# Performance work log

Measured on AMD Instinct MI355X. Metric: run time of the kernel, lower is better.

The kernel has to match this reference:

```python
import jax, jax.numpy as jnp
import numpy as np

H = 4      # hidden_size
L = 5      # num_layers
IN = 1     # input_size
B = 1024   # batch
T = 2048   # seq_len


def setup_inputs() -> dict:
    key = jax.random.key(0)
    ks = jax.random.split(key, 6)
    s = 1.0 / np.sqrt(H)  # PyTorch LSTM init: U(-1/sqrt(H), 1/sqrt(H))
    u = lambda k, shape: jax.random.uniform(k, shape, jnp.float32, -s, s)
    return {
        "x": jax.random.normal(ks[0], (B, T, IN), jnp.float32),
        "w_ih0": u(ks[1], (4 * H, IN)),          # layer 0 input weights
        "w_ih_rest": u(ks[2], (L - 1, 4 * H, H)),  # layers 1..L-1 input weights
        "w_hh": u(ks[3], (L, 4 * H, H)),
        "b_ih": u(ks[4], (L, 4 * H)),
        "b_hh": u(ks[5], (L, 4 * H)),
    }


def _lstm_layer(seq, w_ih, w_hh, b_ih, b_hh):
    # seq: [T, B, in] -> outputs [T, B, H], final hidden [B, H]
    # Precompute input contributions for all timesteps (one big GEMM).
    gx = jnp.einsum('tbi,gi->tbg', seq, w_ih) + b_ih + b_hh  # [T, B, 4H]
    h0 = jnp.zeros((seq.shape[1], H), seq.dtype)
    c0 = h0

    def step(carry, g_t):
        h, c = carry
        g = g_t + h @ w_hh.T                      # [B, 4H]
        i, f, gc, o = jnp.split(g, 4, axis=-1)    # PyTorch gate order i,f,g,o
        i = jax.nn.sigmoid(i)
        f = jax.nn.sigmoid(f)
        o = jax.nn.sigmoid(o)
        c = f * c + i * jnp.tanh(gc)
        h = o * jnp.tanh(c)
        return (h, c), h

    (hT, _), out = jax.lax.scan(step, (h0, c0), gx)
    return out, hT


def reference(x, w_ih0, w_ih_rest, w_hh, b_ih, b_hh):
    seq = jnp.transpose(x, (1, 0, 2))  # batch_first -> time-major [T, B, IN]
    out, hT = _lstm_layer(seq, w_ih0, w_hh[0], b_ih[0], b_hh[0])
    for l in range(L - 1):  # fixed small layer count; structural loop is fine
        out, hT = _lstm_layer(out, w_ih_rest[l], w_hh[l + 1], b_ih[l + 1], b_hh[l + 1])
    # final hidden state of the last (top) layer == rnn_hidden_states[-1]
    return hT  # [B, H]
```

## Files before the change

kernel.cpp:

```cpp
#include <hip/hip_runtime.h>
#include <stdint.h>


#define T_LEN   2048
#define NLAYER  5
#define CHUNK   32
#define NCHUNK  (T_LEN / CHUNK)
#define NPHASE  (NCHUNK + NLAYER - 1)

template <int CTRL>
__device__ __forceinline__ float dppmov(float x) {
  int v = __builtin_amdgcn_mov_dpp(__float_as_int(x), CTRL, 0xF, 0xF, true);
  return __int_as_float(v);
}

template <bool STORE>
__device__ __forceinline__ void lstm_step(
    float gxv, const float* whh, float k1, float k0,
    float& hr0, float& hr1, float& hr2, float& hr3, float& c,
    float* __restrict__ slot)
{
  const float LOG2E = 1.4426950408889634f;

  float t01 = fmaf(whh[0], hr0, gxv);
  t01 = fmaf(whh[1], hr1, t01);
  float t23 = whh[2] * hr2;
  t23 = fmaf(whh[3], hr3, t23);
  const float acc = t01 + t23;

  const float E = __builtin_amdgcn_exp2f(acc);
  const float A = 1.f + E;
  const float R = __builtin_amdgcn_rcpf(A);
  const float act = fmaf(k1, R, k0);

  const float iv = dppmov<0x00>(act);
  const float fv = dppmov<0x55>(act);
  const float gv = dppmov<0xAA>(act);
  const float ov = dppmov<0xFF>(act);
  const float ov2 = ov + ov;
  const float ovm = -ov;

  c = fmaf(fv, c, iv * gv);
  const float ct = c * (-2.0f * LOG2E);
  const float E2 = __builtin_amdgcn_exp2f(ct);
  const float A2 = 1.f + E2;
  const float R2 = __builtin_amdgcn_rcpf(A2);
  const float h  = fmaf(ov2, R2, ovm);

  hr0 = h;
  hr1 = dppmov<0x124>(h);
  hr2 = dppmov<0x128>(h);
  hr3 = dppmov<0x12C>(h);

  if (STORE) *slot = h;
}

__global__ void __launch_bounds__(64 * NLAYER, 1) lstm_pipe(
    const float* __restrict__ x,
    const float* __restrict__ w_ih0,
    const float* __restrict__ w_ih_rest,
    const float* __restrict__ w_hh,
    const float* __restrict__ b_ih,
    const float* __restrict__ b_hh,
    float* __restrict__ out)
{
  const int tid  = threadIdx.x;
  const int l    = tid >> 6;
  const int lane = tid & 63;
  const int q    = lane & 15;
  const int el   = lane >> 4;
  const int e    = blockIdx.x * 4 + el;
  const int gt   = q & 3;
  const int j    = q >> 2;
  const int r    = gt * 4 + j;

  const float LOG2E = 1.4426950408889634f;
  const float s  = (gt == 2) ? (-2.0f * LOG2E) : (-LOG2E);
  const float k1 = (gt == 2) ? 2.0f : 1.0f;
  const float k0 = (gt == 2) ? -1.0f : 0.0f;

  float whh[4];
  float wih[4] = {0.f, 0.f, 0.f, 0.f};
  #pragma unroll
  for (int m = 0; m < 4; ++m) {
    const int k = (j - m) & 3;
    whh[m] = w_hh[l * 64 + r * 4 + k] * s;
  }
  if (l > 0) {
    #pragma unroll
    for (int m = 0; m < 4; ++m) {
      const int k = (j - m) & 3;
      wih[m] = w_ih_rest[(l - 1) * 64 + r * 4 + k] * s;
    }
  }
  float wx = 0.f;
  if (l == 0) wx = w_ih0[r] * s;
  const float bias = (b_ih[l * 16 + r] + b_hh[l * 16 + r]) * s;

  float hr0 = 0.f, hr1 = 0.f, hr2 = 0.f, hr3 = 0.f;
  float c = 0.f;

  __shared__ float buf[NLAYER - 1][2][CHUNK][4][16];

  float gx[CHUNK];
  float xcur[CHUNK];

  if (l == 0) {
    #pragma unroll
    for (int tc = 0; tc < CHUNK; ++tc) xcur[tc] = x[e * T_LEN + tc];
  }

  for (int p = 0; p < NPHASE; ++p) {
    const int n = p - l;
    if (n >= 0 && n < NCHUNK) {
      const int par = n & 1;

      if (l == 0) {
        #pragma unroll
        for (int tc = 0; tc < CHUNK; ++tc)
          gx[tc] = fmaf(wx, xcur[tc], bias);
        if (n + 1 < NCHUNK) {
          #pragma unroll
          for (int tc = 0; tc < CHUNK; ++tc)
            xcur[tc] = x[e * T_LEN + (n + 1) * CHUNK + tc];
        }
      } else {
        #pragma unroll
        for (int tc = 0; tc < CHUNK; ++tc) {
          const float a0 = buf[l - 1][par][tc][el][q];
          const float a1 = dppmov<0x124>(a0);
          const float a2 = dppmov<0x128>(a0);
          const float a3 = dppmov<0x12C>(a0);
          float acc = fmaf(wih[0], a0, bias);
          acc = fmaf(wih[1], a1, acc);
          float acc2 = wih[2] * a2;
          acc2 = fmaf(wih[3], a3, acc2);
          gx[tc] = acc + acc2;
        }
      }

      __builtin_amdgcn_s_setprio(1);
      if (l < NLAYER - 1) {
        float* slotbase = &buf[l][par][0][el][q];
        #pragma unroll
        for (int tc = 0; tc < CHUNK; ++tc)
          lstm_step<true>(gx[tc], whh, k1, k0, hr0, hr1, hr2, hr3, c,
                          slotbase + tc * 64);
      } else {
        #pragma unroll
        for (int tc = 0; tc < CHUNK; ++tc)
          lstm_step<false>(gx[tc], whh, k1, k0, hr0, hr1, hr2, hr3, c,
                           nullptr);
      }
      __builtin_amdgcn_s_setprio(0);

      if (l == NLAYER - 1 && n == NCHUNK - 1 && gt == 0) out[e * 4 + j] = hr0;
    }
    __syncthreads();
  }
}

extern "C" void kernel_launch(void* const* d_in, const int* in_sizes, int n_in,
                              void* d_out, int out_size, void* d_ws, size_t ws_size,
                              hipStream_t stream) {
  const float* x     = (const float*)d_in[0];
  const float* wih0  = (const float*)d_in[1];
  const float* wrest = (const float*)d_in[2];
  const float* whh   = (const float*)d_in[3];
  const float* bih   = (const float*)d_in[4];
  const float* bhh   = (const float*)d_in[5];
  float* out = (float*)d_out;

  dim3 grid(256);
  dim3 block(64 * NLAYER);
  lstm_pipe<<<grid, block, 0, stream>>>(x, wih0, wrest, whh, bih, bhh, out);
}
```

Before: 299.9 us.

## Compute next layer's input projection in producer step and pad LDS rows

Result: faster. 287.4 us (-4.2%).

```diff
diff --git a/kernel.cpp b/kernel.cpp
--- a/kernel.cpp
+++ b/kernel.cpp
@@ -7,6 +7,7 @@
 #define CHUNK   32
 #define NCHUNK  (T_LEN / CHUNK)
 #define NPHASE  (NCHUNK + NLAYER - 1)
+#define ROWSTR  33
 
 template <int CTRL>
 __device__ __forceinline__ float dppmov(float x) {
@@ -14,9 +15,10 @@
   return __int_as_float(v);
 }
 
-template <bool STORE>
+template <bool PUSH>
 __device__ __forceinline__ void lstm_step(
     float gxv, const float* whh, float k1, float k0,
+    const float* wnx, float bnx,
     float& hr0, float& hr1, float& hr2, float& hr3, float& c,
     float* __restrict__ slot)
 {
@@ -52,7 +54,13 @@
   hr2 = dppmov<0x128>(h);
   hr3 = dppmov<0x12C>(h);
 
-  if (STORE) *slot = h;
+  if (PUSH) {
+    float g = fmaf(wnx[0], hr0, bnx);
+    g = fmaf(wnx[1], hr1, g);
+    float g2 = wnx[2] * hr2;
+    g2 = fmaf(wnx[3], hr3, g2);
+    *slot = g + g2;
+  }
 }
 
 __global__ void __launch_bounds__(64 * NLAYER, 1) lstm_pipe(
@@ -80,27 +88,29 @@
   const float k0 = (gt == 2) ? -1.0f : 0.0f;
 
   float whh[4];
-  float wih[4] = {0.f, 0.f, 0.f, 0.f};
   #pragma unroll
-  for (int m = 0; m < 4; ++m) {
-    const int k = (j - m) & 3;
-    whh[m] = w_hh[l * 64 + r * 4 + k] * s;
+  for (int m = 0; m < 4; ++m)
+    whh[m] = w_hh[l * 64 + r * 4 + ((j - m) & 3)] * s;
+
+  float wnx[4] = {0.f, 0.f, 0.f, 0.f};
+  float bnx = 0.f;
+  if (l < NLAYER - 1) {
+    #pragma unroll
+    for (int m = 0; m < 4; ++m)
+      wnx[m] = w_ih_rest[l * 64 + r * 4 + ((j - m) & 3)] * s;
+    bnx = (b_ih[(l + 1) * 16 + r] + b_hh[(l + 1) * 16 + r]) * s;
   }
-  if (l > 0) {
-    #pragma unroll
-    for (int m = 0; m < 4; ++m) {
-      const int k = (j - m) & 3;
-      wih[m] = w_ih_rest[(l - 1) * 64 + r * 4 + k] * s;
-    }
+
+  float wx = 0.f, bias0 = 0.f;
+  if (l == 0) {
+    wx = w_ih0[r] * s;
+    bias0 = (b_ih[r] + b_hh[r]) * s;
   }
-  float wx = 0.f;
-  if (l == 0) wx = w_ih0[r] * s;
-  const float bias = (b_ih[l * 16 + r] + b_hh[l * 16 + r]) * s;
 
   float hr0 = 0.f, hr1 = 0.f, hr2 = 0.f, hr3 = 0.f;
   float c = 0.f;
 
-  __shared__ float buf[NLAYER - 1][2][CHUNK][4][16];
+  __shared__ float buf[NLAYER - 1][2][64][ROWSTR];
 
   float gx[CHUNK];
   float xcur[CHUNK];
@@ -118,46 +128,37 @@
       if (l == 0) {
         #pragma unroll
         for (int tc = 0; tc < CHUNK; ++tc)
-          gx[tc] = fmaf(wx, xcur[tc], bias);
+          gx[tc] = fmaf(wx, xcur[tc], bias0);
         if (n + 1 < NCHUNK) {
           #pragma unroll
           for (int tc = 0; tc < CHUNK; ++tc)
             xcur[tc] = x[e * T_LEN + (n + 1) * CHUNK + tc];
         }
       } else {
+        const float* row = &buf[l - 1][par][lane][0];
         #pragma unroll
-        for (int tc = 0; tc < CHUNK; ++tc) {
-          const float a0 = buf[l - 1][par][tc][el][q];
-          const float a1 = dppmov<0x124>(a0);
-          const float a2 = dppmov<0x128>(a0);
-          const float a3 = dppmov<0x12C>(a0);
-          float acc = fmaf(wih[0], a0, bias);
-          acc = fmaf(wih[1], a1, acc);
-          float acc2 = wih[2] * a2;
-          acc2 = fmaf(wih[3], a3, acc2);
-          gx[tc] = acc + acc2;
-        }
+        for (int tc = 0; tc < CHUNK; ++tc) gx[tc] = row[tc];
       }
 
       __builtin_amdgcn_s_setprio(1);
       if (l < NLAYER - 1) {
-        float* slotbase = &buf[l][par][0][el][q];
+        float* slot = &buf[l][par][lane][0];
         #pragma unroll
         for (int tc = 0; tc < CHUNK; ++tc)
-          lstm_step<true>(gx[tc], whh, k1, k0, hr0, hr1, hr2, hr3, c,
-                          slotbase + tc * 64);
+          lstm_step<true>(gx[tc], whh, k1, k0, wnx, bnx,
+                          hr0, hr1, hr2, hr3, c, slot + tc);
       } else {
         #pragma unroll
         for (int tc = 0; tc < CHUNK; ++tc)
-          lstm_step<false>(gx[tc], whh, k1, k0, hr0, hr1, hr2, hr3, c,
-                           nullptr);
+          lstm_step<false>(gx[tc], whh, k1, k0, nullptr, 0.f,
+                           hr0, hr1, hr2, hr3, c, nullptr);
       }
       __builtin_amdgcn_s_setprio(0);
-
-      if (l == NLAYER - 1 && n == NCHUNK - 1 && gt == 0) out[e * 4 + j] = hr0;
     }
     __syncthreads();
   }
+
+  if (l == NLAYER - 1 && gt == 0) out[e * 4 + j] = hr0;
 }
 
 extern "C" void kernel_launch(void* const* d_in, const int* in_sizes, int n_in,
```
